# Performance work log

Measured on AMD Instinct MI355X. Metric: run time of the kernel, lower is better.

Reference implementation:

```python
import jax, jax.numpy as jnp
import numpy as np

HEADS = 8


def setup_inputs() -> dict:
    key = jax.random.key(0)
    ks = jax.random.split(key, 6)
    B, N, D = 4, 2048, 512
    return {
        "x": jax.random.normal(ks[0], (B, N, D), dtype=jnp.float32),
        "pos": jax.random.uniform(ks[1], (B, N, 3), dtype=jnp.float32),
        "qkv_w": jax.random.normal(ks[2], (3 * D, D), dtype=jnp.float32) * 0.02,
        "qkv_b": jax.random.normal(ks[3], (3 * D,), dtype=jnp.float32) * 0.02,
        "out_w": jax.random.normal(ks[4], (D, D), dtype=jnp.float32) * 0.02,
        "out_b": jax.random.normal(ks[5], (D,), dtype=jnp.float32) * 0.02,
    }


def reference(x, pos, qkv_w, qkv_b, out_w, out_b):
    B, N, D = x.shape
    H = HEADS
    Dh = D // H
    scale = D ** (-0.5)  # NOTE: original uses full dim, not head dim

    # QKV projection -> [3, B, H, N, Dh]
    qkv = (x @ qkv_w.T + qkv_b).reshape(B, N, 3, H, Dh).transpose(2, 0, 3, 1, 4)
    q, k, v = qkv[0], qkv[1], qkv[2]

    # partial 3D RoPE on first 6 head dims (3 axis pairs)
    theta = pos * jnp.pi                    # [B, N, 3]
    sin = jnp.sin(theta)[:, None]           # [B, 1, N, 3] broadcasts over heads
    cos = jnp.cos(theta)[:, None]

    def rotate(t):
        x_rot = t[..., :6]
        x1 = x_rot[..., 0::2]               # [B, H, N, 3]
        x2 = x_rot[..., 1::2]
        return jnp.concatenate(
            [x1 * cos - x2 * sin, x1 * sin + x2 * cos, t[..., 6:]], axis=-1
        )

    q = rotate(q)
    k = rotate(k)

    attn = jax.nn.softmax(jnp.einsum("bhqd,bhkd->bhqk", q, k) * scale, axis=-1)
    out = jnp.einsum("bhqk,bhkd->bhqd", attn, v)          # [B, H, N, Dh]
    out = out.transpose(0, 2, 1, 3).reshape(B, N, D)
    return out @ out_w.T + out_b
```

## Files before the change

### kernel.cpp

```cpp
#include <hip/hip_runtime.h>
#include <stdint.h>

typedef __attribute__((ext_vector_type(4))) float f32x4;
typedef __attribute__((ext_vector_type(16))) float f32x16;
typedef __attribute__((ext_vector_type(8))) short bf16x8;
typedef __attribute__((ext_vector_type(4))) unsigned short u16x4;

__device__ __forceinline__ unsigned short f2bf(float f) {
    unsigned int u = __builtin_bit_cast(unsigned int, f);
    u += 0x7fffu + ((u >> 16) & 1u);
    return (unsigned short)(u >> 16);
}
__device__ __forceinline__ float bf2f(unsigned short s) {
    unsigned int u = ((unsigned int)s) << 16;
    return __builtin_bit_cast(float, u);
}
__device__ __forceinline__ float fexp2(float x) {
#if __has_builtin(__builtin_amdgcn_exp2f)
    return __builtin_amdgcn_exp2f(x);
#else
    return exp2f(x);
#endif
}
__device__ __forceinline__ unsigned int cvt_pk_bf16(float lo, float hi) {
    unsigned int r;
    asm("v_cvt_pk_bf16_f32 %0, %1, %2" : "=v"(r) : "v"(lo), "v"(hi));
    return r;
}

__global__ void k_cvt3(const float* __restrict__ x,
                       const float* __restrict__ w1,
                       const float* __restrict__ w2,
                       unsigned short* __restrict__ out) {
    const int C1 = 1048576;
    const int C2 = 196608;
    int i = blockIdx.x * blockDim.x + threadIdx.x;
    f32x4 v;
    if (i < C1)            v = ((const f32x4*)x)[i];
    else if (i < C1 + C2)  v = ((const f32x4*)w1)[i - C1];
    else                   v = ((const f32x4*)w2)[i - C1 - C2];
    u16x4 o;
    o.x = f2bf(v.x); o.y = f2bf(v.y); o.z = f2bf(v.z); o.w = f2bf(v.w);
    ((u16x4*)out)[i] = o;
}

template<int OUT_BF16>
__global__ __launch_bounds__(256, 3)
void k_gemm_nt(const unsigned short* __restrict__ A,
               const unsigned short* __restrict__ Bm,
               const float* __restrict__ bias,
               void* __restrict__ Cout, int M, int N, int K, int colblocks) {
    __shared__ unsigned short As[3][128 * 32];
    __shared__ unsigned short Bs[3][128 * 32];
    const int tid = threadIdx.x;
    const int lane = tid & 63;
    const int w = tid >> 6;
    const int wr = (w >> 1) * 64, wc = (w & 1) * 64;
    const int g = lane >> 4, fr = lane & 15;

    const int bid = blockIdx.x;
    const int xcd = bid & 7, loc = bid >> 3;
    const int rowb = xcd * 8 + (loc & 7);
    const int colb = loc >> 3;
    (void)colblocks;

    f32x4 acc[4][4];
#pragma unroll
    for (int i = 0; i < 4; ++i)
#pragma unroll
        for (int j = 0; j < 4; ++j) acc[i][j] = f32x4{0.f, 0.f, 0.f, 0.f};

    const int srow16 = lane >> 2;
    const int schunk = ((lane & 3) ^ (srow16 & 3)) * 8;
    const int sA = w, sB = w + 4;
    const unsigned short* Aseg0 = A + (size_t)(rowb * 128 + sA * 16 + srow16) * K + schunk;
    const unsigned short* Aseg1 = A + (size_t)(rowb * 128 + sB * 16 + srow16) * K + schunk;
    const unsigned short* Bseg0 = Bm + (size_t)(colb * 128 + sA * 16 + srow16) * K + schunk;
    const unsigned short* Bseg1 = Bm + (size_t)(colb * 128 + sB * 16 + srow16) * K + schunk;

    auto stage = [&](int bsel, int k0) {
        char* la = (char*)&As[bsel][0];
        char* lb = (char*)&Bs[bsel][0];
        __builtin_amdgcn_global_load_lds((const __attribute__((address_space(1))) void*)(Aseg0 + k0),
                                         (__attribute__((address_space(3))) void*)(la + sA * 1024), 16, 0, 0);
        __builtin_amdgcn_global_load_lds((const __attribute__((address_space(1))) void*)(Aseg1 + k0),
                                         (__attribute__((address_space(3))) void*)(la + sB * 1024), 16, 0, 0);
        __builtin_amdgcn_global_load_lds((const __attribute__((address_space(1))) void*)(Bseg0 + k0),
                                         (__attribute__((address_space(3))) void*)(lb + sA * 1024), 16, 0, 0);
        __builtin_amdgcn_global_load_lds((const __attribute__((address_space(1))) void*)(Bseg1 + k0),
                                         (__attribute__((address_space(3))) void*)(lb + sB * 1024), 16, 0, 0);
    };
    auto compute = [&](int bsel) {
        bf16x8 af[4], bfv[4];
        const int rc = (g ^ (fr & 3)) * 8;
#pragma unroll
        for (int mi = 0; mi < 4; ++mi)
            af[mi] = *(const bf16x8*)&As[bsel][(wr + mi * 16 + fr) * 32 + rc];
#pragma unroll
        for (int ni = 0; ni < 4; ++ni)
            bfv[ni] = *(const bf16x8*)&Bs[bsel][(wc + ni * 16 + fr) * 32 + rc];
        __builtin_amdgcn_s_setprio(1);
#pragma unroll
        for (int mi = 0; mi < 4; ++mi)
#pragma unroll
            for (int ni = 0; ni < 4; ++ni)
                acc[mi][ni] = __builtin_amdgcn_mfma_f32_16x16x32_bf16(af[mi], bfv[ni], acc[mi][ni], 0, 0, 0);
        __builtin_amdgcn_s_setprio(0);
    };

    const int nt = K >> 5;
    stage(0, 0);
    stage(1, 32);
    int cur = 0;
#pragma unroll 1
    for (int t = 0; t < nt; ++t) {
        if (t < nt - 1) asm volatile("s_waitcnt vmcnt(4)" ::: "memory");
        else            asm volatile("s_waitcnt vmcnt(0)" ::: "memory");
        __builtin_amdgcn_s_barrier();
        compute(cur);
        if (t + 2 < nt) {
            int nxt = cur + 2; if (nxt >= 3) nxt -= 3;
            stage(nxt, (t + 2) << 5);
        }
        cur = (cur + 1 == 3) ? 0 : cur + 1;
    }

#pragma unroll
    for (int mi = 0; mi < 4; ++mi) {
#pragma unroll
        for (int ni = 0; ni < 4; ++ni) {
            int row = rowb * 128 + wr + mi * 16 + g * 4;
            int col = colb * 128 + wc + ni * 16 + fr;
            float bz = bias[col];
#pragma unroll
            for (int r = 0; r < 4; ++r) {
                float v = acc[mi][ni][r] + bz;
                if (OUT_BF16) ((unsigned short*)Cout)[(size_t)(row + r) * N + col] = f2bf(v);
                else          ((float*)Cout)[(size_t)(row + r) * N + col] = v;
            }
        }
    }
}

__global__ void k_rotary(const unsigned short* __restrict__ qkv,
                         const float* __restrict__ pos,
                         unsigned short* __restrict__ Qb,
                         unsigned short* __restrict__ Kb,
                         unsigned short* __restrict__ VT) {
    const float PI = 3.14159265358979323846f;
    const float QS = 0.04419417382415922f * 1.44269504088896341f;
    int cid = blockIdx.x * 256 + threadIdx.x;
    int s = cid >> 19;
    int r = cid & 524287;
    if (s < 2) {
        int m = r >> 6, c = r & 63;
        int h = c >> 3, dc = c & 7;
        int b = m >> 11, n = m & 2047;
        bf16x8 v = *(const bf16x8*)&qkv[m * 1536 + s * 512 + c * 8];
        float f[8];
#pragma unroll
        for (int i = 0; i < 8; ++i) f[i] = bf2f((unsigned short)v[i]);
        if (dc == 0) {
            float nf[6];
#pragma unroll
            for (int j = 0; j < 3; ++j) {
                float th = pos[m * 3 + j] * PI;
                float sn = __sinf(th), cs = __cosf(th);
                float x1 = f[2 * j], x2 = f[2 * j + 1];
                nf[j] = x1 * cs - x2 * sn;
                nf[3 + j] = x1 * sn + x2 * cs;
            }
#pragma unroll
            for (int j = 0; j < 6; ++j) f[j] = nf[j];
        }
        if (s == 0) {
#pragma unroll
            for (int i = 0; i < 8; ++i) f[i] *= QS;
        }
        bf16x8 o;
#pragma unroll
        for (int i = 0; i < 8; ++i) o[i] = (short)f2bf(f[i]);
        unsigned short* dst = (s == 0) ? Qb : Kb;
        *(bf16x8*)&dst[((size_t)(b * 8 + h) * 2048 + n) * 64 + dc * 8] = o;
    } else {
        int cd = r >> 13;
        int m = r & 8191;
        int b = m >> 11, n = m & 2047;
        int h = cd >> 3, d8 = (cd & 7) * 8;
        bf16x8 v = *(const bf16x8*)&qkv[m * 1536 + 1024 + cd * 8];
        int q2 = (n >> 2) & 3;
        int np = n + (q2 == 1 ? 4 : (q2 == 2 ? -4 : 0));
        size_t base = ((size_t)(b * 8 + h) * 64 + d8) * 2048 + np;
#pragma unroll
        for (int i = 0; i < 8; ++i) VT[base + (size_t)i * 2048] = (unsigned short)v[i];
    }
}

__global__ __launch_bounds__(512, 4)
void k_attn(const unsigned short* __restrict__ Qb,
            const unsigned short* __restrict__ Kb,
            const unsigned short* __restrict__ VT,
            unsigned short* __restrict__ Ob) {
    __shared__ unsigned short smem[2][2][2][4096];
    const int tid = threadIdx.x, lane = tid & 63, w = tid >> 6;
    const int wl = w & 3, half = w >> 2;
    const int l31 = lane & 31, hi = lane >> 5;
    const int bid = blockIdx.x;
    const int bh = (bid & 7) * 4 + ((bid >> 3) >> 4);
    const int qb = (bid >> 3) & 15;
    const int b = bh >> 3, h = bh & 7;
    const int qr0 = qb * 128 + wl * 32;
    const unsigned short* Q = Qb + (size_t)bh * 2048 * 64;
    const unsigned short* K = Kb + (size_t)bh * 2048 * 64;
    const unsigned short* V = VT + (size_t)bh * 64 * 2048;
    const int thalf = half * 16;

    const int srow8 = lane >> 3;
    const int swc = ((lane & 7) ^ srow8) << 3;
    const int sA = wl, sB = wl + 4;

    bf16x8 bq[4];
#pragma unroll
    for (int ds = 0; ds < 4; ++ds)
        bq[ds] = *(const bf16x8*)&Q[(size_t)(qr0 + l31) * 64 + ds * 16 + hi * 8];

    f32x16 oT0, oT1;
#pragma unroll
    for (int i = 0; i < 16; ++i) { oT0[i] = 0.f; oT1[i] = 0.f; }
    float lpart = 0.f;

    auto stage = [&](int bsel, int t) {
        const int kv0 = t * 64;
        const unsigned short* k0 = K + (size_t)(kv0 + sA * 8 + srow8) * 64 + swc;
        const unsigned short* k1 = K + (size_t)(kv0 + sB * 8 + srow8) * 64 + swc;
        const unsigned short* v0 = V + (size_t)(sA * 8 + srow8) * 2048 + kv0 + swc;
        const unsigned short* v1 = V + (size_t)(sB * 8 + srow8) * 2048 + kv0 + swc;
        char* dk = (char*)&smem[half][0][bsel][0];
        char* dv = (char*)&smem[half][1][bsel][0];
        __builtin_amdgcn_global_load_lds((const __attribute__((address_space(1))) void*)k0,
                                         (__attribute__((address_space(3))) void*)(dk + sA * 1024), 16, 0, 0);
        __builtin_amdgcn_global_load_lds((const __attribute__((address_space(1))) void*)k1,
                                         (__attribute__((address_space(3))) void*)(dk + sB * 1024), 16, 0, 0);
        __builtin_amdgcn_global_load_lds((const __attribute__((address_space(1))) void*)v0,
                                         (__attribute__((address_space(3))) void*)(dv + sA * 1024), 16, 0, 0);
        __builtin_amdgcn_global_load_lds((const __attribute__((address_space(1))) void*)v1,
                                         (__attribute__((address_space(3))) void*)(dv + sB * 1024), 16, 0, 0);
    };

    auto pack8 = [&](const float* p) -> bf16x8 {
        union { unsigned int u[4]; bf16x8 v; } c;
        c.u[0] = cvt_pk_bf16(p[0], p[1]);
        c.u[1] = cvt_pk_bf16(p[2], p[3]);
        c.u[2] = cvt_pk_bf16(p[4], p[5]);
        c.u[3] = cvt_pk_bf16(p[6], p[7]);
        return c.v;
    };

    auto compute = [&](int bsel) {
        const unsigned short* KsC = &smem[half][0][bsel][0];
        const unsigned short* VtC = &smem[half][1][bsel][0];
        f32x16 s0, s1;
#pragma unroll
        for (int i = 0; i < 16; ++i) { s0[i] = 0.f; s1[i] = 0.f; }
        __builtin_amdgcn_s_setprio(1);
#pragma unroll
        for (int ds = 0; ds < 4; ++ds) {
            const int c = ((((ds << 1) | hi) ^ (l31 & 7)) << 3);
            bf16x8 ka0 = *(const bf16x8*)&KsC[l31 * 64 + c];
            bf16x8 ka1 = *(const bf16x8*)&KsC[(32 + l31) * 64 + c];
            s0 = __builtin_amdgcn_mfma_f32_32x32x16_bf16(ka0, bq[ds], s0, 0, 0, 0);
            s1 = __builtin_amdgcn_mfma_f32_32x32x16_bf16(ka1, bq[ds], s1, 0, 0, 0);
        }
        __builtin_amdgcn_s_setprio(0);
        float p0[16], p1[16];
        float lsum = 0.f;
#pragma unroll
        for (int r = 0; r < 16; ++r) {
            p0[r] = fexp2(s0[r]);
            p1[r] = fexp2(s1[r]);
            lsum += p0[r] + p1[r];
        }
        lpart += lsum;
        bf16x8 pb0 = pack8(p0);
        bf16x8 pb1 = pack8(p0 + 8);
        bf16x8 pb2 = pack8(p1);
        bf16x8 pb3 = pack8(p1 + 8);
        __builtin_amdgcn_s_setprio(1);
#pragma unroll
        for (int kb = 0; kb < 4; ++kb) {
            const int c = ((((kb << 1) | hi) ^ (l31 & 7)) << 3);
            bf16x8 av0 = *(const bf16x8*)&VtC[l31 * 64 + c];
            bf16x8 av1 = *(const bf16x8*)&VtC[(32 + l31) * 64 + c];
            bf16x8 pbk = (kb == 0) ? pb0 : (kb == 1) ? pb1 : (kb == 2) ? pb2 : pb3;
            oT0 = __builtin_amdgcn_mfma_f32_32x32x16_bf16(av0, pbk, oT0, 0, 0, 0);
            oT1 = __builtin_amdgcn_mfma_f32_32x32x16_bf16(av1, pbk, oT1, 0, 0, 0);
        }
        __builtin_amdgcn_s_setprio(0);
    };

    stage(0, thalf);
    asm volatile("s_waitcnt vmcnt(0)" ::: "memory");
    __builtin_amdgcn_s_barrier();
    int cur = 0;
#pragma unroll 1
    for (int t = 0; t < 16; ++t) {
        if (t < 15) stage(cur ^ 1, thalf + t + 1);
        compute(cur);
        if (t < 15) {
            asm volatile("s_waitcnt vmcnt(0)" ::: "memory");
            __builtin_amdgcn_s_barrier();
        }
        cur ^= 1;
    }

    __syncthreads();
    float* mrg = (float*)&smem[0][0][0][0];
    float* slot = mrg + (size_t)(wl * 64 + lane) * 33;
    if (half) {
#pragma unroll
        for (int i = 0; i < 16; ++i) { slot[i] = oT0[i]; slot[16 + i] = oT1[i]; }
        slot[32] = lpart;
    }
    __syncthreads();
    if (!half) {
#pragma unroll
        for (int i = 0; i < 16; ++i) { oT0[i] += slot[i]; oT1[i] += slot[16 + i]; }
        float lf = lpart + slot[32];
        lf += __shfl_xor(lf, 32, 64);
        float il = 1.f / lf;
        size_t rowbase = (size_t)(b * 2048 + qr0 + l31) * 512 + h * 64;
#pragma unroll
        for (int grp = 0; grp < 4; ++grp) {
            u16x4 o0, o1;
#pragma unroll
            for (int i = 0; i < 4; ++i) {
                o0[i] = f2bf(oT0[grp * 4 + i] * il);
                o1[i] = f2bf(oT1[grp * 4 + i] * il);
            }
            int dv0 = grp * 8 + 4 * hi;
            *(u16x4*)&Ob[rowbase + dv0] = o0;
            *(u16x4*)&Ob[rowbase + 32 + dv0] = o1;
        }
    }
}

extern "C" void kernel_launch(void* const* d_in, const int* in_sizes, int n_in,
                              void* d_out, int out_size, void* d_ws, size_t ws_size,
                              hipStream_t stream) {
    const float* x     = (const float*)d_in[0];
    const float* pos   = (const float*)d_in[1];
    const float* qkv_w = (const float*)d_in[2];
    const float* qkv_b = (const float*)d_in[3];
    const float* out_w = (const float*)d_in[4];
    const float* out_b = (const float*)d_in[5];
    float* out = (float*)d_out;

    unsigned short* Xb   = (unsigned short*)d_ws;
    unsigned short* W1b  = Xb   + (size_t)8192 * 512;
    unsigned short* W2b  = W1b  + (size_t)1536 * 512;
    unsigned short* QKVb = W2b  + (size_t)512 * 512;
    unsigned short* Qb   = QKVb + (size_t)8192 * 1536;
    unsigned short* Kb   = Qb   + (size_t)4194304;
    unsigned short* VTb  = Kb   + (size_t)4194304;
    unsigned short* Ob   = VTb  + (size_t)4194304;

    k_cvt3<<<5120, 256, 0, stream>>>(x, qkv_w, out_w, Xb);
    k_gemm_nt<1><<<768, 256, 0, stream>>>(Xb, W1b, qkv_b, QKVb, 8192, 1536, 512, 12);
    k_rotary<<<6144, 256, 0, stream>>>(QKVb, pos, Qb, Kb, VTb);
    k_attn<<<512, 512, 0, stream>>>(Qb, Kb, VTb, Ob);
    k_gemm_nt<0><<<256, 256, 0, stream>>>(Ob, W2b, out_b, out, 8192, 512, 512, 4);
}
```

Measured before the change: 93.34 us.

## Fuse RoPE, Q scaling and Q/K/V head-split layout into QKV GEMM epilogue

Removes the separate rotary kernel by applying RoPE, the Q softmax scale, and the head-major Q/K and transposed V scatter directly in the QKV GEMM epilogue. Lane shuffles fetch the paired rotation inputs within each 16-column fragment. This avoids writing and re-reading the full bf16 QKV intermediate and saves one launch. In exchange the epilogue stores are scalar and scattered (strided 2-byte writes for Q/K and 8-byte writes into VT), so write coalescing may suffer.

After: 85.60 us. -8.3%, faster.

```diff
diff --git a/kernel.cpp b/kernel.cpp
--- a/kernel.cpp
+++ b/kernel.cpp
@@ -44,12 +44,17 @@
     ((u16x4*)out)[i] = o;
 }
 
-template<int OUT_BF16>
 __global__ __launch_bounds__(256, 3)
-void k_gemm_nt(const unsigned short* __restrict__ A,
-               const unsigned short* __restrict__ Bm,
-               const float* __restrict__ bias,
-               void* __restrict__ Cout, int M, int N, int K, int colblocks) {
+void k_gemm_qkv(const unsigned short* __restrict__ A,
+                const unsigned short* __restrict__ Bm,
+                const float* __restrict__ bias,
+                const float* __restrict__ pos,
+                unsigned short* __restrict__ Qb,
+                unsigned short* __restrict__ Kb,
+                unsigned short* __restrict__ VT) {
+    const float PI = 3.14159265358979323846f;
+    const float QS = 0.04419417382415922f * 1.44269504088896341f;
+    const int K = 512, N = 1536;
     __shared__ unsigned short As[3][128 * 32];
     __shared__ unsigned short Bs[3][128 * 32];
     const int tid = threadIdx.x;
@@ -62,7 +67,6 @@
     const int xcd = bid & 7, loc = bid >> 3;
     const int rowb = xcd * 8 + (loc & 7);
     const int colb = loc >> 3;
-    (void)colblocks;
 
     f32x4 acc[4][4];
 #pragma unroll
@@ -125,6 +129,8 @@
         cur = (cur + 1 == 3) ? 0 : cur + 1;
     }
 
+    const int jrot = (fr < 3) ? fr : ((fr < 6) ? fr - 3 : 0);
+    const int shbase = lane & 48;
 #pragma unroll
     for (int mi = 0; mi < 4; ++mi) {
 #pragma unroll
@@ -132,67 +138,136 @@
             int row = rowb * 128 + wr + mi * 16 + g * 4;
             int col = colb * 128 + wc + ni * 16 + fr;
             float bz = bias[col];
-#pragma unroll
-            for (int r = 0; r < 4; ++r) {
-                float v = acc[mi][ni][r] + bz;
-                if (OUT_BF16) ((unsigned short*)Cout)[(size_t)(row + r) * N + col] = f2bf(v);
-                else          ((float*)Cout)[(size_t)(row + r) * N + col] = v;
+            float v[4];
+#pragma unroll
+            for (int r = 0; r < 4; ++r) v[r] = acc[mi][ni][r] + bz;
+            int b = row >> 11, n = row & 2047;
+            if (colb < 8) {
+                const int isQ = (colb < 4);
+                int qcol = isQ ? col : col - 512;
+                int h = qcol >> 6, dh = qcol & 63;
+                if (ni == 0) {
+#pragma unroll
+                    for (int r = 0; r < 4; ++r) {
+                        float x1 = __shfl(v[r], shbase + 2 * jrot, 64);
+                        float x2 = __shfl(v[r], shbase + 2 * jrot + 1, 64);
+                        if (fr < 6) {
+                            float th = pos[(row + r) * 3 + jrot] * PI;
+                            float sn = __sinf(th), cs = __cosf(th);
+                            v[r] = (fr < 3) ? (x1 * cs - x2 * sn) : (x1 * sn + x2 * cs);
+                        }
+                    }
+                }
+                float qs = isQ ? QS : 1.f;
+                unsigned short* dst = isQ ? Qb : Kb;
+                size_t rb = (size_t)(b * 8 + h) * 2048 + n;
+#pragma unroll
+                for (int r = 0; r < 4; ++r)
+                    dst[(rb + r) * 64 + dh] = f2bf(v[r] * qs);
+            } else {
+                int vcol = col - 1024;
+                int h = vcol >> 6, dh = vcol & 63;
+                int q2 = (n >> 2) & 3;
+                int np = n + (q2 == 1 ? 4 : (q2 == 2 ? -4 : 0));
+                u16x4 o;
+#pragma unroll
+                for (int r = 0; r < 4; ++r) o[r] = f2bf(v[r]);
+                *(u16x4*)&VT[((size_t)(b * 8 + h) * 64 + dh) * 2048 + np] = o;
             }
         }
     }
 }
 
-__global__ void k_rotary(const unsigned short* __restrict__ qkv,
-                         const float* __restrict__ pos,
-                         unsigned short* __restrict__ Qb,
-                         unsigned short* __restrict__ Kb,
-                         unsigned short* __restrict__ VT) {
-    const float PI = 3.14159265358979323846f;
-    const float QS = 0.04419417382415922f * 1.44269504088896341f;
-    int cid = blockIdx.x * 256 + threadIdx.x;
-    int s = cid >> 19;
-    int r = cid & 524287;
-    if (s < 2) {
-        int m = r >> 6, c = r & 63;
-        int h = c >> 3, dc = c & 7;
-        int b = m >> 11, n = m & 2047;
-        bf16x8 v = *(const bf16x8*)&qkv[m * 1536 + s * 512 + c * 8];
-        float f[8];
-#pragma unroll
-        for (int i = 0; i < 8; ++i) f[i] = bf2f((unsigned short)v[i]);
-        if (dc == 0) {
-            float nf[6];
-#pragma unroll
-            for (int j = 0; j < 3; ++j) {
-                float th = pos[m * 3 + j] * PI;
-                float sn = __sinf(th), cs = __cosf(th);
-                float x1 = f[2 * j], x2 = f[2 * j + 1];
-                nf[j] = x1 * cs - x2 * sn;
-                nf[3 + j] = x1 * sn + x2 * cs;
-            }
-#pragma unroll
-            for (int j = 0; j < 6; ++j) f[j] = nf[j];
-        }
-        if (s == 0) {
-#pragma unroll
-            for (int i = 0; i < 8; ++i) f[i] *= QS;
-        }
-        bf16x8 o;
-#pragma unroll
-        for (int i = 0; i < 8; ++i) o[i] = (short)f2bf(f[i]);
-        unsigned short* dst = (s == 0) ? Qb : Kb;
-        *(bf16x8*)&dst[((size_t)(b * 8 + h) * 2048 + n) * 64 + dc * 8] = o;
-    } else {
-        int cd = r >> 13;
-        int m = r & 8191;
-        int b = m >> 11, n = m & 2047;
-        int h = cd >> 3, d8 = (cd & 7) * 8;
-        bf16x8 v = *(const bf16x8*)&qkv[m * 1536 + 1024 + cd * 8];
-        int q2 = (n >> 2) & 3;
-        int np = n + (q2 == 1 ? 4 : (q2 == 2 ? -4 : 0));
-        size_t base = ((size_t)(b * 8 + h) * 64 + d8) * 2048 + np;
-#pragma unroll
-        for (int i = 0; i < 8; ++i) VT[base + (size_t)i * 2048] = (unsigned short)v[i];
+__global__ __launch_bounds__(256, 3)
+void k_gemm_out(const unsigned short* __restrict__ A,
+                const unsigned short* __restrict__ Bm,
+                const float* __restrict__ bias,
+                float* __restrict__ Cout, int M, int N, int K) {
+    __shared__ unsigned short As[3][128 * 32];
+    __shared__ unsigned short Bs[3][128 * 32];
+    const int tid = threadIdx.x;
+    const int lane = tid & 63;
+    const int w = tid >> 6;
+    const int wr = (w >> 1) * 64, wc = (w & 1) * 64;
+    const int g = lane >> 4, fr = lane & 15;
+
+    const int bid = blockIdx.x;
+    const int xcd = bid & 7, loc = bid >> 3;
+    const int rowb = xcd * 8 + (loc & 7);
+    const int colb = loc >> 3;
+
+    f32x4 acc[4][4];
+#pragma unroll
+    for (int i = 0; i < 4; ++i)
+#pragma unroll
+        for (int j = 0; j < 4; ++j) acc[i][j] = f32x4{0.f, 0.f, 0.f, 0.f};
+
+    const int srow16 = lane >> 2;
+    const int schunk = ((lane & 3) ^ (srow16 & 3)) * 8;
+    const int sA = w, sB = w + 4;
+    const unsigned short* Aseg0 = A + (size_t)(rowb * 128 + sA * 16 + srow16) * K + schunk;
+    const unsigned short* Aseg1 = A + (size_t)(rowb * 128 + sB * 16 + srow16) * K + schunk;
+    const unsigned short* Bseg0 = Bm + (size_t)(colb * 128 + sA * 16 + srow16) * K + schunk;
+    const unsigned short* Bseg1 = Bm + (size_t)(colb * 128 + sB * 16 + srow16) * K + schunk;
+
+    auto stage = [&](int bsel, int k0) {
+        char* la = (char*)&As[bsel][0];
+        char* lb = (char*)&Bs[bsel][0];
+        __builtin_amdgcn_global_load_lds((const __attribute__((address_space(1))) void*)(Aseg0 + k0),
+                                         (__attribute__((address_space(3))) void*)(la + sA * 1024), 16, 0, 0);
+        __builtin_amdgcn_global_load_lds((const __attribute__((address_space(1))) void*)(Aseg1 + k0),
+                                         (__attribute__((address_space(3))) void*)(la + sB * 1024), 16, 0, 0);
+        __builtin_amdgcn_global_load_lds((const __attribute__((address_space(1))) void*)(Bseg0 + k0),
+                                         (__attribute__((address_space(3))) void*)(lb + sA * 1024), 16, 0, 0);
+        __builtin_amdgcn_global_load_lds((const __attribute__((address_space(1))) void*)(Bseg1 + k0),
+                                         (__attribute__((address_space(3))) void*)(lb + sB * 1024), 16, 0, 0);
+    };
+    auto compute = [&](int bsel) {
+        bf16x8 af[4], bfv[4];
+        const int rc = (g ^ (fr & 3)) * 8;
+#pragma unroll
+        for (int mi = 0; mi < 4; ++mi)
+            af[mi] = *(const bf16x8*)&As[bsel][(wr + mi * 16 + fr) * 32 + rc];
+#pragma unroll
+        for (int ni = 0; ni < 4; ++ni)
+            bfv[ni] = *(const bf16x8*)&Bs[bsel][(wc + ni * 16 + fr) * 32 + rc];
+        __builtin_amdgcn_s_setprio(1);
+#pragma unroll
+        for (int mi = 0; mi < 4; ++mi)
+#pragma unroll
+            for (int ni = 0; ni < 4; ++ni)
+                acc[mi][ni] = __builtin_amdgcn_mfma_f32_16x16x32_bf16(af[mi], bfv[ni], acc[mi][ni], 0, 0, 0);
+        __builtin_amdgcn_s_setprio(0);
+    };
+
+    const int nt = K >> 5;
+    stage(0, 0);
+    stage(1, 32);
+    int cur = 0;
+#pragma unroll 1
+    for (int t = 0; t < nt; ++t) {
+        if (t < nt - 1) asm volatile("s_waitcnt vmcnt(4)" ::: "memory");
+        else            asm volatile("s_waitcnt vmcnt(0)" ::: "memory");
+        __builtin_amdgcn_s_barrier();
+        compute(cur);
+        if (t + 2 < nt) {
+            int nxt = cur + 2; if (nxt >= 3) nxt -= 3;
+            stage(nxt, (t + 2) << 5);
+        }
+        cur = (cur + 1 == 3) ? 0 : cur + 1;
+    }
+
+#pragma unroll
+    for (int mi = 0; mi < 4; ++mi) {
+#pragma unroll
+        for (int ni = 0; ni < 4; ++ni) {
+            int row = rowb * 128 + wr + mi * 16 + g * 4;
+            int col = colb * 128 + wc + ni * 16 + fr;
+            float bz = bias[col];
+#pragma unroll
+            for (int r = 0; r < 4; ++r)
+                Cout[(size_t)(row + r) * N + col] = acc[mi][ni][r] + bz;
+        }
     }
 }
 
@@ -358,15 +433,13 @@
     unsigned short* Xb   = (unsigned short*)d_ws;
     unsigned short* W1b  = Xb   + (size_t)8192 * 512;
     unsigned short* W2b  = W1b  + (size_t)1536 * 512;
-    unsigned short* QKVb = W2b  + (size_t)512 * 512;
-    unsigned short* Qb   = QKVb + (size_t)8192 * 1536;
+    unsigned short* Qb   = W2b  + (size_t)512 * 512;
     unsigned short* Kb   = Qb   + (size_t)4194304;
     unsigned short* VTb  = Kb   + (size_t)4194304;
     unsigned short* Ob   = VTb  + (size_t)4194304;
 
     k_cvt3<<<5120, 256, 0, stream>>>(x, qkv_w, out_w, Xb);
-    k_gemm_nt<1><<<768, 256, 0, stream>>>(Xb, W1b, qkv_b, QKVb, 8192, 1536, 512, 12);
-    k_rotary<<<6144, 256, 0, stream>>>(QKVb, pos, Qb, Kb, VTb);
+    k_gemm_qkv<<<768, 256, 0, stream>>>(Xb, W1b, qkv_b, pos, Qb, Kb, VTb);
     k_attn<<<512, 512, 0, stream>>>(Qb, Kb, VTb, Ob);
-    k_gemm_nt<0><<<256, 256, 0, stream>>>(Ob, W2b, out_b, out, 8192, 512, 512, 4);
-}
+    k_gemm_out<<<256, 256, 0, stream>>>(Ob, W2b, out_b, out, 8192, 512, 512);
+}
```
